# Kernel tuning notes

Hardware: AMD Instinct MI355X
Metric: run time of the kernel (lower is better)

## Reference

```python
import jax, jax.numpy as jnp
import numpy as np

N_EMBED = 2048
N_HEAD = 16
HEAD_DIM = N_EMBED // N_HEAD  # 128


def setup_inputs() -> dict:
    key = jax.random.key(0)
    k1, k2, k3 = jax.random.split(key, 3)
    B, S = 2, 2048
    x = jax.random.normal(k1, (B, S, N_EMBED), dtype=jnp.float32)
    # torch Linear weight [out,in]; store transposed for x @ W
    scale_attn = 1.0 / np.sqrt(N_EMBED)
    w_attn = jax.random.normal(k2, (N_EMBED, (N_HEAD + 2) * HEAD_DIM), dtype=jnp.float32) * scale_attn
    w_out = jax.random.normal(k3, (N_EMBED, N_EMBED), dtype=jnp.float32) * scale_attn
    return {"x": x, "w_attn": w_attn, "w_out": w_out}


def reference(x, w_attn, w_out):
    B, S, E = x.shape
    H, D = N_HEAD, HEAD_DIM
    qkv = x @ w_attn                               # [B,S,(H+2)*D]
    q, k, v = jnp.split(qkv, [E, E + D], axis=2)   # [B,S,E], [B,S,D], [B,S,D]
    q = q.reshape(B, S, H, D).transpose(0, 2, 1, 3)  # [B,H,S,D]
    # single shared K/V head (MQA)
    scores = jnp.einsum("bhsd,btd->bhst", q, k) * (D ** -0.5)  # [B,H,S,S]
    p = jax.nn.softmax(scores, axis=-1)
    attn = jnp.einsum("bhst,btd->bhsd", p, v)      # [B,H,S,D]
    attn = attn.transpose(0, 2, 1, 3).reshape(B, S, E)
    return attn @ w_out
```

## Files before the change

### kernel.cpp

```cpp
#include <hip/hip_runtime.h>
#include <hip/hip_bf16.h>

typedef __attribute__((ext_vector_type(8))) short short8;
typedef __attribute__((ext_vector_type(4))) float f32x4;

#define GLOBAL_AS __attribute__((address_space(1)))
#define LDS_AS    __attribute__((address_space(3)))

__device__ __forceinline__ unsigned short f2bf(float f) {
    union { float f; unsigned int u; } v; v.f = f;
    unsigned int r = v.u + 0x7FFFu + ((v.u >> 16) & 1u);
    return (unsigned short)(r >> 16);
}

__device__ __forceinline__ unsigned int pk_bf16(float a, float b) {
    union { __hip_bfloat162 h; unsigned int u; } c;
    c.h = __float22bfloat162_rn(float2{a, b});
    return c.u;
}

__device__ __forceinline__ short8 cvt8v(float4 a, float4 b) {
    union { short8 s; unsigned int u[4]; } c;
    c.u[0] = pk_bf16(a.x, a.y); c.u[1] = pk_bf16(a.z, a.w);
    c.u[2] = pk_bf16(b.x, b.y); c.u[3] = pk_bf16(b.z, b.w);
    return c.s;
}

__device__ __forceinline__ void async_ld16(const unsigned short* g, unsigned short* l) {
    __builtin_amdgcn_global_load_lds((const GLOBAL_AS unsigned int*)g,
                                     (LDS_AS unsigned int*)l, 16, 0, 0);
}

__global__ __launch_bounds__(256) void transpose_cvt(
    const float* __restrict__ src, unsigned short* __restrict__ dst, int K, int N)
{
    __shared__ unsigned short t[64][72];
    const int tid = threadIdx.x;
    const int n0 = blockIdx.x * 64, k0 = blockIdx.y * 64;
    #pragma unroll
    for (int it = 0; it < 4; ++it) {
        int r = it * 16 + (tid >> 4);
        int c = (tid & 15) * 4;
        float4 v = *(const float4*)(src + (size_t)(k0 + r) * N + n0 + c);
        t[r][c] = f2bf(v.x); t[r][c + 1] = f2bf(v.y);
        t[r][c + 2] = f2bf(v.z); t[r][c + 3] = f2bf(v.w);
    }
    __syncthreads();
    const int nr = tid >> 2, kg = (tid & 3) * 16;
    short8 o0, o1;
    #pragma unroll
    for (int j = 0; j < 8; ++j) { o0[j] = (short)t[kg + j][nr]; o1[j] = (short)t[kg + 8 + j][nr]; }
    *(short8*)(dst + (size_t)(n0 + nr) * K + k0 + kg) = o0;
    *(short8*)(dst + (size_t)(n0 + nr) * K + k0 + kg + 8) = o1;
}

template<bool A_F32, bool OUT_F32>
__global__ __launch_bounds__(256, 3) void gemm_bt(
    const void* __restrict__ Av, const unsigned short* __restrict__ Bt,
    void* __restrict__ Cv, int M, int N, int K)
{
    constexpr int APAD = A_F32 ? 40 : 32;
    __shared__ __align__(16) unsigned short As[128][APAD];
    __shared__ __align__(16) unsigned short Bs[128][32];

    const int tid = threadIdx.x, lane = tid & 63, w = tid >> 6;
    const int quad = lane >> 4, l15 = lane & 15;
    const int m0 = blockIdx.y * 128, n0 = blockIdx.x * 128;
    const int rw = (w >> 1) * 64, cw = (w & 1) * 64;

    const float* Af = (const float*)Av;
    const unsigned short* Ab = (const unsigned short*)Av;

    const f32x4 zero = {0.f, 0.f, 0.f, 0.f};
    f32x4 acc[4][4];
    #pragma unroll
    for (int i = 0; i < 4; ++i)
        #pragma unroll
        for (int j = 0; j < 4; ++j) acc[i][j] = zero;

    const int srow = lane >> 2;
    const int scol = (lane & 3) * 8;
    const int ar = tid >> 1, ak = (tid & 1) * 16;

    float4 p0, p1, p2, p3;
    const float* pA;

    if constexpr (A_F32) {
        pA = Af + (size_t)(m0 + ar) * K + ak;
        p0 = *(const float4*)(pA);     p1 = *(const float4*)(pA + 4);
        p2 = *(const float4*)(pA + 8); p3 = *(const float4*)(pA + 12);
        *(short8*)&As[ar][ak]     = cvt8v(p0, p1);
        *(short8*)&As[ar][ak + 8] = cvt8v(p2, p3);
        if (K > 32) {
            p0 = *(const float4*)(pA + 32); p1 = *(const float4*)(pA + 36);
            p2 = *(const float4*)(pA + 40); p3 = *(const float4*)(pA + 44);
        }
    } else {
        #pragma unroll
        for (int c = 0; c < 2; ++c)
            async_ld16(Ab + (size_t)(m0 + w * 32 + c * 16 + srow) * K + scol,
                       &As[w * 32 + c * 16][0]);
    }
    #pragma unroll
    for (int c = 0; c < 2; ++c)
        async_ld16(Bt + (size_t)(n0 + w * 32 + c * 16 + srow) * K + scol,
                   &Bs[w * 32 + c * 16][0]);

    for (int k0 = 0; k0 < K; k0 += 32) {
        __syncthreads();

        short8 af[4], bf2[4];
        #pragma unroll
        for (int i = 0; i < 4; ++i)
            af[i] = *(const short8*)&As[rw + i * 16 + l15][quad * 8];
        #pragma unroll
        for (int j = 0; j < 4; ++j)
            bf2[j] = *(const short8*)&Bs[cw + j * 16 + l15][quad * 8];
        __syncthreads();

        if (k0 + 32 < K) {
            if constexpr (A_F32) {
                *(short8*)&As[ar][ak]     = cvt8v(p0, p1);
                *(short8*)&As[ar][ak + 8] = cvt8v(p2, p3);
                if (k0 + 64 < K) {
                    p0 = *(const float4*)(pA + k0 + 64); p1 = *(const float4*)(pA + k0 + 68);
                    p2 = *(const float4*)(pA + k0 + 72); p3 = *(const float4*)(pA + k0 + 76);
                }
            } else {
                #pragma unroll
                for (int c = 0; c < 2; ++c)
                    async_ld16(Ab + (size_t)(m0 + w * 32 + c * 16 + srow) * K + k0 + 32 + scol,
                               &As[w * 32 + c * 16][0]);
            }
            #pragma unroll
            for (int c = 0; c < 2; ++c)
                async_ld16(Bt + (size_t)(n0 + w * 32 + c * 16 + srow) * K + k0 + 32 + scol,
                           &Bs[w * 32 + c * 16][0]);
        }

        #pragma unroll
        for (int i = 0; i < 4; ++i)
            #pragma unroll
            for (int j = 0; j < 4; ++j)
                acc[i][j] = __builtin_amdgcn_mfma_f32_16x16x32_bf16(af[i], bf2[j], acc[i][j], 0, 0, 0);
    }

    #pragma unroll
    for (int i = 0; i < 4; ++i) {
        const int row = m0 + rw + i * 16 + quad * 4;
        #pragma unroll
        for (int j = 0; j < 4; ++j) {
            const int col = n0 + cw + j * 16 + l15;
            #pragma unroll
            for (int r = 0; r < 4; ++r) {
                if constexpr (OUT_F32)
                    ((float*)Cv)[(size_t)(row + r) * N + col] = acc[i][j][r];
                else
                    ((unsigned short*)Cv)[(size_t)(row + r) * N + col] = f2bf(acc[i][j][r]);
            }
        }
    }
}

__global__ __launch_bounds__(256) void mqa_flash(
    const unsigned short* __restrict__ qkv,
    unsigned short* __restrict__ attn)
{
    const int S = 2048, QKVW = 2304;
    __shared__ __align__(16) union {
        struct {
            unsigned short Ks[2][32][136];
            unsigned short VT[2][144][44];
        } s;
        unsigned short T[4][32][136];
    } sm;

    const int tid = threadIdx.x, lane = tid & 63, w = tid >> 6;
    const int quad = lane >> 4, l15 = lane & 15;
    const int bid = blockIdx.x;
    const int qb = bid & 15;
    const int h  = (bid >> 4) & 15;
    const int b  = bid >> 8;

    for (int i = tid; i < 2 * 16 * 32; i += 256)
        sm.s.VT[i >> 9][128 + ((i >> 5) & 15)][i & 31] = 0x3F80;

    const unsigned short* base = qkv + (size_t)b * S * QKVW;

    short8 qf[2][4];
    #pragma unroll
    for (int sub = 0; sub < 2; ++sub) {
        const int row = qb * 128 + w * 32 + sub * 16 + l15;
        #pragma unroll
        for (int ds = 0; ds < 4; ++ds)
            qf[sub][ds] = *(const short8*)(base + (size_t)row * QKVW + h * 128 + ds * 32 + quad * 8);
    }

    const f32x4 zero = {0.f, 0.f, 0.f, 0.f};
    f32x4 o[2][9];
    #pragma unroll
    for (int sub = 0; sub < 2; ++sub)
        #pragma unroll
        for (int d = 0; d < 9; ++d) o[sub][d] = zero;

    const int krow = tid & 31, kdg = tid >> 5;
    const int kpr  = ((krow & 1) << 4) | (krow >> 1);
    const int vkp  = tid & 15, vdg = tid >> 4;

    const unsigned short* kp = base + (size_t)krow * QKVW + 2048 + kdg * 16;
    const unsigned short* vp = base + (size_t)(2 * vkp) * QKVW + 2176 + vdg * 8;

    short8 k0v = *(const short8*)kp;
    short8 k1v = *(const short8*)(kp + 8);
    short8 v0v = *(const short8*)vp;
    short8 v1v = *(const short8*)(vp + QKVW);

    for (int kb = 0; kb < S; kb += 32) {
        const int p = (kb >> 5) & 1;

        *(short8*)(&sm.s.Ks[p][kpr][kdg * 16]) = k0v;
        *(short8*)(&sm.s.Ks[p][kpr][kdg * 16 + 8]) = k1v;
        #pragma unroll
        for (int j = 0; j < 8; ++j) {
            unsigned int pkv = (unsigned int)(unsigned short)v0v[j]
                             | ((unsigned int)(unsigned short)v1v[j] << 16);
            *(unsigned int*)(&sm.s.VT[p][vdg * 8 + j][vkp * 2]) = pkv;
        }

        if (kb + 32 < S) {
            kp += 32 * QKVW; vp += 32 * QKVW;
            k0v = *(const short8*)kp;
            k1v = *(const short8*)(kp + 8);
            v0v = *(const short8*)vp;
            v1v = *(const short8*)(vp + QKVW);
        }

        __syncthreads();

        __builtin_amdgcn_s_setprio(1);

        f32x4 sc[2][2];
        sc[0][0] = zero; sc[0][1] = zero; sc[1][0] = zero; sc[1][1] = zero;
        #pragma unroll
        for (int ds = 0; ds < 4; ++ds) {
            short8 kf0 = *(const short8*)(&sm.s.Ks[p][l15][ds * 32 + quad * 8]);
            short8 kf1 = *(const short8*)(&sm.s.Ks[p][16 + l15][ds * 32 + quad * 8]);
            #pragma unroll
            for (int sub = 0; sub < 2; ++sub) {
                sc[sub][0] = __builtin_amdgcn_mfma_f32_16x16x32_bf16(kf0, qf[sub][ds], sc[sub][0], 0, 0, 0);
                sc[sub][1] = __builtin_amdgcn_mfma_f32_16x16x32_bf16(kf1, qf[sub][ds], sc[sub][1], 0, 0, 0);
            }
        }

        const float scale = 0.08838834764831845f;
        short8 pf[2];
        #pragma unroll
        for (int sub = 0; sub < 2; ++sub) {
            union { short8 sv; unsigned int u[4]; } c;
            #pragma unroll
            for (int r = 0; r < 4; ++r) {
                float e0 = __expf(fmaf(sc[sub][0][r], scale, -12.f));
                float e1 = __expf(fmaf(sc[sub][1][r], scale, -12.f));
                c.u[r] = pk_bf16(e0, e1);
            }
            pf[sub] = c.sv;
        }

        #pragma unroll
        for (int dsub = 0; dsub < 9; ++dsub) {
            short8 vf = *(const short8*)(&sm.s.VT[p][dsub * 16 + l15][quad * 8]);
            o[0][dsub] = __builtin_amdgcn_mfma_f32_16x16x32_bf16(vf, pf[0], o[0][dsub], 0, 0, 0);
            o[1][dsub] = __builtin_amdgcn_mfma_f32_16x16x32_bf16(vf, pf[1], o[1][dsub], 0, 0, 0);
        }

        __builtin_amdgcn_s_setprio(0);
    }

    __syncthreads();

    #pragma unroll
    for (int sub = 0; sub < 2; ++sub) {
        const float inv = 1.0f / o[sub][8][0];
        #pragma unroll
        for (int dsub = 0; dsub < 8; ++dsub) {
            unsigned int lo = pk_bf16(o[sub][dsub][0] * inv, o[sub][dsub][1] * inv);
            unsigned int hi = pk_bf16(o[sub][dsub][2] * inv, o[sub][dsub][3] * inv);
            unsigned int* dst = (unsigned int*)&sm.T[w][sub * 16 + l15][dsub * 16 + quad * 4];
            dst[0] = lo; dst[1] = hi;
        }
    }
    __syncthreads();

    const size_t rowbase = (size_t)b * S + qb * 128 + w * 32;
    #pragma unroll
    for (int pass = 0; pass < 8; ++pass) {
        const int row = pass * 4 + quad;
        short8 ov = *(const short8*)(&sm.T[w][row][l15 * 8]);
        *(short8*)(&attn[(rowbase + row) * 2048 + h * 128 + l15 * 8]) = ov;
    }
}

extern "C" void kernel_launch(void* const* d_in, const int* in_sizes, int n_in,
                              void* d_out, int out_size, void* d_ws, size_t ws_size,
                              hipStream_t stream)
{
    const float* x     = (const float*)d_in[0];
    const float* wattn = (const float*)d_in[1];
    const float* wout  = (const float*)d_in[2];
    float* out = (float*)d_out;

    unsigned short* ws = (unsigned short*)d_ws;
    unsigned short* qkv    = ws;
    unsigned short* woutT  = ws;
    unsigned short* wattnT = ws + (size_t)9437184;
    unsigned short* attn   = ws + (size_t)9437184;

    transpose_cvt<<<dim3(2304 / 64, 2048 / 64), 256, 0, stream>>>(wattn, wattnT, 2048, 2304);
    gemm_bt<true, false><<<dim3(2304 / 128, 4096 / 128), 256, 0, stream>>>(
        x, wattnT, qkv, 4096, 2304, 2048);
    mqa_flash<<<dim3(2 * 16 * 16), 256, 0, stream>>>(qkv, attn);
    transpose_cvt<<<dim3(2048 / 64, 2048 / 64), 256, 0, stream>>>(wout, woutT, 2048, 2048);
    gemm_bt<false, true><<<dim3(2048 / 128, 4096 / 128), 256, 0, stream>>>(
        attn, woutT, out, 4096, 2048, 2048);
}
```

Measured before the change: 319.1 us.

## Double GEMM K-tile to 64 and add XCD-aware block remapping

Raises the GEMM K-step from 32 to 64, so each iteration loads twice as much A and B into shared memory and issues two MFMAs per accumulator. This halves the number of barriers and loop iterations over K. It also remaps linear block IDs in strides of 8, so that consecutive tiles go to the same XCD and L2 reuse improves. In exchange, shared-memory use and register pressure go up, with eight float4 prefetch registers in the fp32-A path, which may lower occupancy. The remap assumes the block count is divisible by 8.

```diff
diff --git a/kernel.cpp b/kernel.cpp
--- a/kernel.cpp
+++ b/kernel.cpp
@@ -59,13 +59,18 @@
     const void* __restrict__ Av, const unsigned short* __restrict__ Bt,
     void* __restrict__ Cv, int M, int N, int K)
 {
-    constexpr int APAD = A_F32 ? 40 : 32;
+    constexpr int APAD = A_F32 ? 72 : 64;
     __shared__ __align__(16) unsigned short As[128][APAD];
-    __shared__ __align__(16) unsigned short Bs[128][32];
+    __shared__ __align__(16) unsigned short Bs[128][64];
 
     const int tid = threadIdx.x, lane = tid & 63, w = tid >> 6;
     const int quad = lane >> 4, l15 = lane & 15;
-    const int m0 = blockIdx.y * 128, n0 = blockIdx.x * 128;
+
+    const int nwg = gridDim.x * gridDim.y;
+    int lin = blockIdx.y * gridDim.x + blockIdx.x;
+    lin = (lin & 7) * (nwg >> 3) + (lin >> 3);
+    const int m0 = (lin / gridDim.x) * 128, n0 = (lin % gridDim.x) * 128;
+
     const int rw = (w >> 1) * 64, cw = (w & 1) * 64;
 
     const float* Af = (const float*)Av;
@@ -78,71 +83,87 @@
         #pragma unroll
         for (int j = 0; j < 4; ++j) acc[i][j] = zero;
 
-    const int srow = lane >> 2;
-    const int scol = (lane & 3) * 8;
-    const int ar = tid >> 1, ak = (tid & 1) * 16;
-
-    float4 p0, p1, p2, p3;
+    const int srow = lane >> 3;
+    const int scol = (lane & 7) * 8;
+    const int ar = tid >> 1, ak = (tid & 1) * 32;
+
+    float4 p0, p1, p2, p3, p4, p5, p6, p7;
     const float* pA;
 
     if constexpr (A_F32) {
         pA = Af + (size_t)(m0 + ar) * K + ak;
-        p0 = *(const float4*)(pA);     p1 = *(const float4*)(pA + 4);
-        p2 = *(const float4*)(pA + 8); p3 = *(const float4*)(pA + 12);
-        *(short8*)&As[ar][ak]     = cvt8v(p0, p1);
-        *(short8*)&As[ar][ak + 8] = cvt8v(p2, p3);
-        if (K > 32) {
-            p0 = *(const float4*)(pA + 32); p1 = *(const float4*)(pA + 36);
-            p2 = *(const float4*)(pA + 40); p3 = *(const float4*)(pA + 44);
+        p0 = *(const float4*)(pA);      p1 = *(const float4*)(pA + 4);
+        p2 = *(const float4*)(pA + 8);  p3 = *(const float4*)(pA + 12);
+        p4 = *(const float4*)(pA + 16); p5 = *(const float4*)(pA + 20);
+        p6 = *(const float4*)(pA + 24); p7 = *(const float4*)(pA + 28);
+        *(short8*)&As[ar][ak]      = cvt8v(p0, p1);
+        *(short8*)&As[ar][ak + 8]  = cvt8v(p2, p3);
+        *(short8*)&As[ar][ak + 16] = cvt8v(p4, p5);
+        *(short8*)&As[ar][ak + 24] = cvt8v(p6, p7);
+        if (K > 64) {
+            p0 = *(const float4*)(pA + 64); p1 = *(const float4*)(pA + 68);
+            p2 = *(const float4*)(pA + 72); p3 = *(const float4*)(pA + 76);
+            p4 = *(const float4*)(pA + 80); p5 = *(const float4*)(pA + 84);
+            p6 = *(const float4*)(pA + 88); p7 = *(const float4*)(pA + 92);
         }
     } else {
         #pragma unroll
-        for (int c = 0; c < 2; ++c)
-            async_ld16(Ab + (size_t)(m0 + w * 32 + c * 16 + srow) * K + scol,
-                       &As[w * 32 + c * 16][0]);
-    }
-    #pragma unroll
-    for (int c = 0; c < 2; ++c)
-        async_ld16(Bt + (size_t)(n0 + w * 32 + c * 16 + srow) * K + scol,
-                   &Bs[w * 32 + c * 16][0]);
-
-    for (int k0 = 0; k0 < K; k0 += 32) {
+        for (int c = 0; c < 4; ++c)
+            async_ld16(Ab + (size_t)(m0 + w * 32 + c * 8 + srow) * K + scol,
+                       &As[w * 32 + c * 8][0]);
+    }
+    #pragma unroll
+    for (int c = 0; c < 4; ++c)
+        async_ld16(Bt + (size_t)(n0 + w * 32 + c * 8 + srow) * K + scol,
+                   &Bs[w * 32 + c * 8][0]);
+
+    for (int k0 = 0; k0 < K; k0 += 64) {
         __syncthreads();
 
-        short8 af[4], bf2[4];
-        #pragma unroll
-        for (int i = 0; i < 4; ++i)
-            af[i] = *(const short8*)&As[rw + i * 16 + l15][quad * 8];
-        #pragma unroll
-        for (int j = 0; j < 4; ++j)
-            bf2[j] = *(const short8*)&Bs[cw + j * 16 + l15][quad * 8];
+        short8 af[4][2], bf2[4][2];
+        #pragma unroll
+        for (int i = 0; i < 4; ++i) {
+            af[i][0] = *(const short8*)&As[rw + i * 16 + l15][quad * 8];
+            af[i][1] = *(const short8*)&As[rw + i * 16 + l15][32 + quad * 8];
+        }
+        #pragma unroll
+        for (int j = 0; j < 4; ++j) {
+            bf2[j][0] = *(const short8*)&Bs[cw + j * 16 + l15][quad * 8];
+            bf2[j][1] = *(const short8*)&Bs[cw + j * 16 + l15][32 + quad * 8];
+        }
         __syncthreads();
 
-        if (k0 + 32 < K) {
+        if (k0 + 64 < K) {
             if constexpr (A_F32) {
-                *(short8*)&As[ar][ak]     = cvt8v(p0, p1);
-                *(short8*)&As[ar][ak + 8] = cvt8v(p2, p3);
-                if (k0 + 64 < K) {
-                    p0 = *(const float4*)(pA + k0 + 64); p1 = *(const float4*)(pA + k0 + 68);
-                    p2 = *(const float4*)(pA + k0 + 72); p3 = *(const float4*)(pA + k0 + 76);
+                *(short8*)&As[ar][ak]      = cvt8v(p0, p1);
+                *(short8*)&As[ar][ak + 8]  = cvt8v(p2, p3);
+                *(short8*)&As[ar][ak + 16] = cvt8v(p4, p5);
+                *(short8*)&As[ar][ak + 24] = cvt8v(p6, p7);
+                if (k0 + 128 < K) {
+                    p0 = *(const float4*)(pA + k0 + 128); p1 = *(const float4*)(pA + k0 + 132);
+                    p2 = *(const float4*)(pA + k0 + 136); p3 = *(const float4*)(pA + k0 + 140);
+                    p4 = *(const float4*)(pA + k0 + 144); p5 = *(const float4*)(pA + k0 + 148);
+                    p6 = *(const float4*)(pA + k0 + 152); p7 = *(const float4*)(pA + k0 + 156);
                 }
             } else {
                 #pragma unroll
-                for (int c = 0; c < 2; ++c)
-                    async_ld16(Ab + (size_t)(m0 + w * 32 + c * 16 + srow) * K + k0 + 32 + scol,
-                               &As[w * 32 + c * 16][0]);
-            }
-            #pragma unroll
-            for (int c = 0; c < 2; ++c)
-                async_ld16(Bt + (size_t)(n0 + w * 32 + c * 16 + srow) * K + k0 + 32 + scol,
-                           &Bs[w * 32 + c * 16][0]);
+                for (int c = 0; c < 4; ++c)
+                    async_ld16(Ab + (size_t)(m0 + w * 32 + c * 8 + srow) * K + k0 + 64 + scol,
+                               &As[w * 32 + c * 8][0]);
+            }
+            #pragma unroll
+            for (int c = 0; c < 4; ++c)
+                async_ld16(Bt + (size_t)(n0 + w * 32 + c * 8 + srow) * K + k0 + 64 + scol,
+                           &Bs[w * 32 + c * 8][0]);
         }
 
         #pragma unroll
         for (int i = 0; i < 4; ++i)
             #pragma unroll
-            for (int j = 0; j < 4; ++j)
-                acc[i][j] = __builtin_amdgcn_mfma_f32_16x16x32_bf16(af[i], bf2[j], acc[i][j], 0, 0, 0);
+            for (int j = 0; j < 4; ++j) {
+                acc[i][j] = __builtin_amdgcn_mfma_f32_16x16x32_bf16(af[i][0], bf2[j][0], acc[i][j], 0, 0, 0);
+                acc[i][j] = __builtin_amdgcn_mfma_f32_16x16x32_bf16(af[i][1], bf2[j][1], acc[i][j], 0, 0, 0);
+            }
     }
 
     #pragma unroll
```

After: 443.8 us. 1.39x slower.
